# Performance work log

Measured on AMD Instinct MI355X. Metric: run time of the kernel, lower is better.

The kernel has to match this reference:

```python
import jax, jax.numpy as jnp
import numpy as np

E4M3_MAX = 448.0
M, K, N = 131072, 512, 512


def _round_to_fp8_e4m3(x):
    # Emulated round-to-nearest E4M3: 3 mantissa bits, exponent in [-7, 8]
    abs_x = jnp.abs(x)
    sign = jnp.sign(x)
    exponent = jnp.clip(jnp.floor(jnp.log2(jnp.maximum(abs_x, 2.0 ** -9))), -7.0, 8.0)
    pow2e = jnp.exp2(exponent)
    mantissa = jnp.round(abs_x / pow2e * 8.0) / 8.0  # jnp.round is half-to-even, matching torch.round
    return sign * mantissa * pow2e


def _quantize_e4m3(x, scale):
    scaled = jnp.clip(x * scale, -E4M3_MAX, E4M3_MAX)
    return _round_to_fp8_e4m3(scaled)


def _dynamic_scale(x):
    # FP8TensorMeta.compute_scale with a single amax in history: max_value / amax * 0.9
    amax = jnp.max(jnp.abs(x))
    return jnp.where(amax > 0, E4M3_MAX / amax * 0.9, 1.0)


def setup_inputs() -> dict:
    key = jax.random.key(0)
    k1, k2, k3 = jax.random.split(key, 3)
    bound = 1.0 / np.sqrt(K)  # kaiming_uniform(a=sqrt(5)) on [N,K] -> U(-1/sqrt(K), 1/sqrt(K))
    x = jax.random.normal(k1, (M, K), dtype=jnp.float32)
    weight = jax.random.uniform(k2, (N, K), dtype=jnp.float32, minval=-bound, maxval=bound)
    bias = jax.random.uniform(k3, (N,), dtype=jnp.float32, minval=-bound, maxval=bound)
    return {"x": x, "weight": weight, "bias": bias}


def reference(x, weight, bias):
    input_scale = _dynamic_scale(x)
    weight_scale = _dynamic_scale(weight)
    x_fp8 = _quantize_e4m3(x, input_scale)          # [M, K]
    w_fp8 = _quantize_e4m3(weight, weight_scale)    # [N, K]
    out = jnp.einsum("mk,nk->mn", x_fp8, w_fp8) + bias  # F.linear
    return out / (input_scale * weight_scale)
```

## Files before the change

kernel.cpp:

```cpp
#include <hip/hip_runtime.h>

typedef unsigned short u16;
typedef unsigned int u32;
typedef __attribute__((ext_vector_type(8))) short short8;
typedef __attribute__((ext_vector_type(4))) float f32x4;

__device__ __forceinline__ u16 quant_bf16(float v, float scale) {
  float sc = v * scale;
  sc = fminf(448.0f, fmaxf(-448.0f, sc));
  u32 b = __float_as_uint(sc);
  u32 sb = (b & 0x7f800000u) + 0x0A000000u;
  sb = sb < 0x46000000u ? 0x46000000u : sb;
  float mg = __uint_as_float(sb);
  float q = (fabsf(sc) + mg) - mg;
  u32 qb = __float_as_uint(q) | (b & 0x80000000u);
  return (u16)(qb >> 16);
}

__device__ __forceinline__ float block_max(float m) {
#pragma unroll
  for (int off = 32; off > 0; off >>= 1)
    m = fmaxf(m, __shfl_down(m, off, 64));
  __shared__ float sm[4];
  int wv = threadIdx.x >> 6;
  if ((threadIdx.x & 63) == 0) sm[wv] = m;
  __syncthreads();
  float r = fmaxf(fmaxf(sm[0], sm[1]), fmaxf(sm[2], sm[3]));
  __syncthreads();
  return r;
}

#define XBLOCKS 2048
#define WBLOCKS 64

__global__ void amax2_kernel(const float4* __restrict__ x, int nx4,
                             const float4* __restrict__ w, int nw4,
                             float* __restrict__ px, float* __restrict__ pw) {
  int bid = blockIdx.x;
  const float4* p;
  int n4, b, nb;
  float* dst;
  if (bid < XBLOCKS) { p = x; n4 = nx4; dst = px; b = bid; nb = XBLOCKS; }
  else { p = w; n4 = nw4; dst = pw; b = bid - XBLOCKS; nb = WBLOCKS; }
  float m = 0.0f;
  int stride = nb * 256;
  for (int i = b * 256 + threadIdx.x; i < n4; i += stride) {
    float4 v = p[i];
    m = fmaxf(m, fmaxf(fmaxf(fabsf(v.x), fabsf(v.y)), fmaxf(fabsf(v.z), fabsf(v.w))));
  }
  m = block_max(m);
  if (threadIdx.x == 0) dst[b] = m;
}

__global__ void scales_kernel(const float* __restrict__ px, const float* __restrict__ pw,
                              float* __restrict__ wsf) {
  int tid = threadIdx.x;
  float mx = 0.0f;
  for (int i = tid; i < XBLOCKS; i += 256) mx = fmaxf(mx, px[i]);
  mx = block_max(mx);
  float mw = tid < WBLOCKS ? pw[tid] : 0.0f;
  mw = block_max(mw);
  if (tid == 0) {
    float sx = mx > 0.0f ? 448.0f / mx * 0.9f : 1.0f;
    float sw = mw > 0.0f ? 448.0f / mw * 0.9f : 1.0f;
    wsf[2] = sx;
    wsf[3] = sw;
    wsf[4] = 1.0f / (sx * sw);
  }
}

__global__ void quant_w_kernel(const float4* __restrict__ w, uint2* __restrict__ wq,
                               const float* __restrict__ wsf) {
  float sw = wsf[3];
  int i = blockIdx.x * blockDim.x + threadIdx.x;
  float4 v = w[i];
  uint2 r;
  r.x = (u32)quant_bf16(v.x, sw) | ((u32)quant_bf16(v.y, sw) << 16);
  r.y = (u32)quant_bf16(v.z, sw) | ((u32)quant_bf16(v.w, sw) << 16);
  wq[i] = r;
}

__global__ void __launch_bounds__(256, 2) gemm_kernel(const float* __restrict__ x,
                                                      const u16* __restrict__ wq,
                                                      const float* __restrict__ bias,
                                                      float* __restrict__ out,
                                                      const float* __restrict__ wsf) {
  __shared__ u16 As[128 * 32];
  __shared__ u16 Bs[256 * 32];
  const int tid = threadIdx.x;
  const int lane = tid & 63;
  const int wv = tid >> 6;
  const int quad = lane >> 4;
  const int lr = lane & 15;

  const int lin = blockIdx.x;
  const int xcd = lin & 7;
  const int jn = (lin >> 3) & 1;
  const int grp = lin >> 4;
  const int m0 = (grp * 8 + xcd) * 128;
  const int n0 = jn * 256;

  const float sx = wsf[2];
  const float inv = wsf[4];
  const int wm = (wv >> 1) * 64;
  const int wn = (wv & 1) * 128;
  const int xrow = tid >> 3;
  const int xcol = (tid & 7) * 4;

  f32x4 acc[4][8] = {};

  for (int kt = 0; kt < 16; ++kt) {
    __syncthreads();
#pragma unroll
    for (int i = 0; i < 4; ++i) {
      const int c = wv + i * 4;
      const int n = c * 16 + (lane >> 2);
      const u16* gp = wq + (size_t)(n0 + n) * 512 + kt * 32 + (lane & 3) * 8;
      u16* lp = &Bs[c * 512 + lane * 8];
      __builtin_amdgcn_global_load_lds((const __attribute__((address_space(1))) u32*)gp,
                                       (__attribute__((address_space(3))) u32*)lp, 16, 0, 0);
    }
#pragma unroll
    for (int s = 0; s < 4; ++s) {
      const int r = s * 32 + xrow;
      const float4 v = *(const float4*)(x + (size_t)(m0 + r) * 512 + kt * 32 + xcol);
      uint2 pk;
      pk.x = (u32)quant_bf16(v.x, sx) | ((u32)quant_bf16(v.y, sx) << 16);
      pk.y = (u32)quant_bf16(v.z, sx) | ((u32)quant_bf16(v.w, sx) << 16);
      *(uint2*)&As[r * 32 + xcol] = pk;
    }
    __syncthreads();
    short8 af[4], bf[8];
#pragma unroll
    for (int mi = 0; mi < 4; ++mi)
      af[mi] = *(const short8*)&As[(wm + mi * 16 + lr) * 32 + quad * 8];
#pragma unroll
    for (int ni = 0; ni < 8; ++ni)
      bf[ni] = *(const short8*)&Bs[(wn + ni * 16 + lr) * 32 + quad * 8];
#pragma unroll
    for (int mi = 0; mi < 4; ++mi)
#pragma unroll
      for (int ni = 0; ni < 8; ++ni)
        acc[mi][ni] = __builtin_amdgcn_mfma_f32_16x16x32_bf16(af[mi], bf[ni], acc[mi][ni], 0, 0, 0);
  }

  float bn[8];
#pragma unroll
  for (int ni = 0; ni < 8; ++ni) bn[ni] = bias[n0 + wn + ni * 16 + lr];
#pragma unroll
  for (int mi = 0; mi < 4; ++mi) {
    const int gr = m0 + wm + mi * 16 + quad * 4;
#pragma unroll
    for (int ni = 0; ni < 8; ++ni) {
      const int gc = n0 + wn + ni * 16 + lr;
#pragma unroll
      for (int j = 0; j < 4; ++j)
        out[(size_t)(gr + j) * 512 + gc] = (acc[mi][ni][j] + bn[ni]) * inv;
    }
  }
}

extern "C" void kernel_launch(void* const* d_in, const int* in_sizes, int n_in,
                              void* d_out, int out_size, void* d_ws, size_t ws_size,
                              hipStream_t stream) {
  const float* x = (const float*)d_in[0];
  const float* w = (const float*)d_in[1];
  const float* bias = (const float*)d_in[2];
  float* out = (float*)d_out;

  const int K = 512, N = 512;
  const int M = in_sizes[0] / K;

  float* ws_f = (float*)d_ws;
  float* px = ws_f + 16;
  float* pw = ws_f + 16 + XBLOCKS;
  u16* wq = (u16*)((char*)d_ws + 16384);

  hipLaunchKernelGGL(amax2_kernel, dim3(XBLOCKS + WBLOCKS), dim3(256), 0, stream,
                     (const float4*)x, (M * K) / 4, (const float4*)w, (N * K) / 4, px, pw);
  hipLaunchKernelGGL(scales_kernel, dim3(1), dim3(256), 0, stream, px, pw, ws_f);
  hipLaunchKernelGGL(quant_w_kernel, dim3((N * K / 4) / 256), dim3(256), 0, stream,
                     (const float4*)w, (uint2*)wq, ws_f);
  hipLaunchKernelGGL(gemm_kernel, dim3((M / 128) * 2), dim3(256), 0, stream,
                     x, wq, bias, out, ws_f);
}
```

Before: 553.4 us.

## Double-buffer GEMM LDS tiles and relayout quantized weights k-chunk-major

```diff
diff --git a/kernel.cpp b/kernel.cpp
--- a/kernel.cpp
+++ b/kernel.cpp
@@ -69,15 +69,21 @@
   }
 }
 
-__global__ void quant_w_kernel(const float4* __restrict__ w, uint2* __restrict__ wq,
+__global__ void quant_w_kernel(const float* __restrict__ w, u16* __restrict__ wq,
                                const float* __restrict__ wsf) {
-  float sw = wsf[3];
-  int i = blockIdx.x * blockDim.x + threadIdx.x;
-  float4 v = w[i];
-  uint2 r;
-  r.x = (u32)quant_bf16(v.x, sw) | ((u32)quant_bf16(v.y, sw) << 16);
-  r.y = (u32)quant_bf16(v.z, sw) | ((u32)quant_bf16(v.w, sw) << 16);
-  wq[i] = r;
+  const float sw = wsf[3];
+  const int id = blockIdx.x * blockDim.x + threadIdx.x;
+  const int kc = id >> 9;
+  const int n = id & 511;
+  const float4* src = (const float4*)(w + (size_t)n * 512 + kc * 8);
+  const float4 a = src[0];
+  const float4 b = src[1];
+  uint4 r;
+  r.x = (u32)quant_bf16(a.x, sw) | ((u32)quant_bf16(a.y, sw) << 16);
+  r.y = (u32)quant_bf16(a.z, sw) | ((u32)quant_bf16(a.w, sw) << 16);
+  r.z = (u32)quant_bf16(b.x, sw) | ((u32)quant_bf16(b.y, sw) << 16);
+  r.w = (u32)quant_bf16(b.z, sw) | ((u32)quant_bf16(b.w, sw) << 16);
+  *(uint4*)&wq[(size_t)kc * 4096 + n * 8] = r;
 }
 
 __global__ void __launch_bounds__(256, 2) gemm_kernel(const float* __restrict__ x,
@@ -85,8 +91,8 @@
                                                       const float* __restrict__ bias,
                                                       float* __restrict__ out,
                                                       const float* __restrict__ wsf) {
-  __shared__ u16 As[128 * 32];
-  __shared__ u16 Bs[256 * 32];
+  __shared__ u16 As[2 * 4096];
+  __shared__ u16 Bs[2 * 8192];
   const int tid = threadIdx.x;
   const int lane = tid & 63;
   const int wv = tid >> 6;
@@ -106,42 +112,64 @@
   const int wn = (wv & 1) * 128;
   const int xrow = tid >> 3;
   const int xcol = (tid & 7) * 4;
+  const int aq = xcol >> 3;
+  const int aoff = xcol & 7;
 
   f32x4 acc[4][8] = {};
-
-  for (int kt = 0; kt < 16; ++kt) {
-    __syncthreads();
+  float4 xr[4];
+
+  auto stageB = [&](int bu, int kt) {
 #pragma unroll
     for (int i = 0; i < 4; ++i) {
-      const int c = wv + i * 4;
-      const int n = c * 16 + (lane >> 2);
-      const u16* gp = wq + (size_t)(n0 + n) * 512 + kt * 32 + (lane & 3) * 8;
-      u16* lp = &Bs[c * 512 + lane * 8];
+      const u16* gp = wq + (size_t)(kt * 4 + wv) * 4096 + (size_t)n0 * 8 + (i * 64 + lane) * 8;
+      u16* lp = &Bs[bu * 8192 + wv * 2048 + (i * 64 + lane) * 8];
       __builtin_amdgcn_global_load_lds((const __attribute__((address_space(1))) u32*)gp,
                                        (__attribute__((address_space(3))) u32*)lp, 16, 0, 0);
     }
+  };
+  auto loadX = [&](int kt) {
 #pragma unroll
     for (int s = 0; s < 4; ++s) {
       const int r = s * 32 + xrow;
-      const float4 v = *(const float4*)(x + (size_t)(m0 + r) * 512 + kt * 32 + xcol);
+      xr[s] = *(const float4*)(x + (size_t)(m0 + r) * 512 + kt * 32 + xcol);
+    }
+  };
+  auto writeA = [&](int bu) {
+#pragma unroll
+    for (int s = 0; s < 4; ++s) {
+      const int r = s * 32 + xrow;
       uint2 pk;
-      pk.x = (u32)quant_bf16(v.x, sx) | ((u32)quant_bf16(v.y, sx) << 16);
-      pk.y = (u32)quant_bf16(v.z, sx) | ((u32)quant_bf16(v.w, sx) << 16);
-      *(uint2*)&As[r * 32 + xcol] = pk;
-    }
-    __syncthreads();
+      pk.x = (u32)quant_bf16(xr[s].x, sx) | ((u32)quant_bf16(xr[s].y, sx) << 16);
+      pk.y = (u32)quant_bf16(xr[s].z, sx) | ((u32)quant_bf16(xr[s].w, sx) << 16);
+      *(uint2*)&As[bu * 4096 + aq * 1024 + r * 8 + aoff] = pk;
+    }
+  };
+
+  stageB(0, 0);
+  loadX(0);
+  writeA(0);
+  __syncthreads();
+
+  for (int kt = 0; kt < 16; ++kt) {
+    const int cur = kt & 1;
+    if (kt < 15) {
+      loadX(kt + 1);
+      stageB(cur ^ 1, kt + 1);
+    }
     short8 af[4], bf[8];
 #pragma unroll
     for (int mi = 0; mi < 4; ++mi)
-      af[mi] = *(const short8*)&As[(wm + mi * 16 + lr) * 32 + quad * 8];
+      af[mi] = *(const short8*)&As[cur * 4096 + quad * 1024 + (wm + mi * 16 + lr) * 8];
 #pragma unroll
     for (int ni = 0; ni < 8; ++ni)
-      bf[ni] = *(const short8*)&Bs[(wn + ni * 16 + lr) * 32 + quad * 8];
+      bf[ni] = *(const short8*)&Bs[cur * 8192 + quad * 2048 + (wn + ni * 16 + lr) * 8];
 #pragma unroll
     for (int mi = 0; mi < 4; ++mi)
 #pragma unroll
       for (int ni = 0; ni < 8; ++ni)
         acc[mi][ni] = __builtin_amdgcn_mfma_f32_16x16x32_bf16(af[mi], bf[ni], acc[mi][ni], 0, 0, 0);
+    if (kt < 15) writeA(cur ^ 1);
+    __syncthreads();
   }
 
   float bn[8];
@@ -179,8 +207,8 @@
   hipLaunchKernelGGL(amax2_kernel, dim3(XBLOCKS + WBLOCKS), dim3(256), 0, stream,
                      (const float4*)x, (M * K) / 4, (const float4*)w, (N * K) / 4, px, pw);
   hipLaunchKernelGGL(scales_kernel, dim3(1), dim3(256), 0, stream, px, pw, ws_f);
-  hipLaunchKernelGGL(quant_w_kernel, dim3((N * K / 4) / 256), dim3(256), 0, stream,
-                     (const float4*)w, (uint2*)wq, ws_f);
+  hipLaunchKernelGGL(quant_w_kernel, dim3((N * K / 8) / 256), dim3(256), 0, stream,
+                     w, wq, ws_f);
   hipLaunchKernelGGL(gemm_kernel, dim3((M / 128) * 2), dim3(256), 0, stream,
                      x, wq, bias, out, ws_f);
 }
```

Measured after the change: 571.7 us. 1.03x slower.
